# Kernel tuning notes

Hardware: AMD Instinct MI355X
Metric: run time of the kernel (lower is better)

The kernel has to match this reference:

```python
import jax, jax.numpy as jnp
import numpy as np

B, F, S, P, E, H = 64, 32, 512, 96, 8, 2048
TOP_K = 2
ALPHA = 10.0
ENT_EPS = 1e-8
CV_EPS = 1e-10


def setup_inputs() -> dict:
    key = jax.random.key(0)
    ks = jax.random.split(key, 8)
    s = 0.02
    return {
        "x": jax.random.normal(ks[0], (B, F, S), dtype=jnp.float32),
        "time_embedding": jax.random.normal(ks[1], (B, F, S), dtype=jnp.float32),
        "Wg": jax.random.normal(ks[2], (S, E), dtype=jnp.float32) * s,
        "bg": jnp.zeros((E,), dtype=jnp.float32),
        "W1": jax.random.normal(ks[3], (E, S, H), dtype=jnp.float32) * s,
        "b1": jnp.zeros((E, H), dtype=jnp.float32),
        "W2": jax.random.normal(ks[4], (E, H, P), dtype=jnp.float32) * s,
        "b2": jnp.zeros((E, P), dtype=jnp.float32),
    }


def _gates(tf, Wg, bg):
    # tf: [F, B, S] -> logits [F, B, E]
    logits = jnp.einsum('fbs,se->fbe', tf, Wg) + bg
    # kthvalue(x, E - top_k + 1) = (E - top_k)-th entry (0-based) of ascending sort = k-th largest
    kth = jnp.sort(logits, axis=-1)[..., E - TOP_K]  # [F, B]
    mask = logits < kth[..., None]
    sm = jax.nn.softmax(logits, axis=-1)
    dec = jnp.where(mask, ALPHA * jnp.log(sm + 1.0), ALPHA * (jnp.exp(sm) - 1.0))
    return jax.nn.softmax(dec, axis=-1)  # [F, B, E]


def reference(x, time_embedding, Wg, bg, W1, b1, W2, b2):
    xf = jnp.transpose(x, (1, 0, 2))               # [F, B, S]
    tf = jnp.transpose(time_embedding, (1, 0, 2))  # [F, B, S]
    gates = _gates(tf, Wg, bg)                     # [F, B, E]

    # all experts on all features (eval mode: dropout = identity)
    h = jax.nn.gelu(jnp.einsum('fbs,esh->febh', xf, W1) + b1[None, :, None, :], approximate=False)
    eo = jnp.einsum('febh,ehp->febp', h, W2) + b2[None, :, None, :]  # [F, E, B, P]
    out = jnp.einsum('fbe,febp->fbp', gates, eo)   # gated weighted sum
    output = jnp.transpose(out, (1, 0, 2))         # [B, F, P]

    # selector loss: cv_squared of importance = gates.sum(batch) expanded over pred_len
    gsum = gates.sum(axis=1)                       # [F, E]
    imp = jnp.broadcast_to(gsum[..., None], (F, E, P)).reshape(F, E * P)
    cv = jnp.var(imp, axis=1, ddof=1) / (jnp.mean(imp, axis=1) ** 2 + CV_EPS)
    selector_loss = jnp.sum(cv)                    # loss_coef = 1.0

    # entropy loss: importance1 = gates.mean(batch) expanded over pred_len
    gmean = gates.mean(axis=1)                     # [F, E]
    imp1 = jnp.broadcast_to(gmean[..., None], (F, E, P))
    entropy_loss = jnp.sum((-imp1 * jnp.log(imp1 + ENT_EPS)).mean(axis=(1, 2)))

    return output, selector_loss, entropy_loss
```

## Files before the change

kernel.cpp:

```cpp
#include <hip/hip_runtime.h>
#include <math.h>

#define B_ 64
#define F_ 32
#define S_ 512
#define P_ 96
#define E_ 8
#define H_ 2048
#define M_ 2048

#define BM 128
#define BH 128
#define BK 64
#define ZSPLIT 4
#define HPZ (H_ / ZSPLIT)
#define NHT (HPZ / BH)
#define NKC (S_ / BK)
#define HPITCH 136

typedef __bf16 bf16x8 __attribute__((ext_vector_type(8)));
typedef __bf16 bf16x4 __attribute__((ext_vector_type(4)));
typedef float f32x4 __attribute__((ext_vector_type(4)));

#define MFMA16(a, b, c) __builtin_amdgcn_mfma_f32_16x16x32_bf16((a), (b), (c), 0, 0, 0)

#define GLL16(gp, lp) __builtin_amdgcn_global_load_lds(                     \
    (const __attribute__((address_space(1))) void*)(gp),                    \
    (__attribute__((address_space(3))) void*)(lp), 16, 0, 0)

__device__ __forceinline__ float fast_gelu(float x) {
  float e = __builtin_amdgcn_exp2f(-2.45546696f * x);
  return x * __builtin_amdgcn_rcpf(1.0f + e);
}

__global__ __launch_bounds__(256) void k_prep_w1(const float* __restrict__ W1,
                                                 __bf16* __restrict__ w1t) {
  __shared__ __align__(16) __bf16 btile[256 * 68];
  const int tid = threadIdx.x;
  int e = blockIdx.x >> 5, hstrip = blockIdx.x & 31;
  const float* src = W1 + (size_t)e * S_ * H_ + hstrip * 64;
  __bf16* dstb = w1t + (size_t)e * H_ * S_ + (size_t)(hstrip * 64) * S_;
#pragma unroll
  for (int pass = 0; pass < 2; ++pass) {
    {
      int rb = tid >> 2;
      int hseg = (tid & 3) * 16;
#pragma unroll
      for (int it = 0; it < 4; ++it) {
        int r = it * 64 + rb;
        const float* srow = src + (size_t)(pass * 256 + r) * H_ + hseg;
#pragma unroll
        for (int k = 0; k < 4; ++k) {
          f32x4 v = *(const f32x4*)(srow + k * 4);
          bf16x4 o = {(__bf16)v[0], (__bf16)v[1], (__bf16)v[2], (__bf16)v[3]};
          *(bf16x4*)&btile[r * 68 + hseg + k * 4] = o;
        }
      }
    }
    __syncthreads();
    {
      int h = tid >> 2;
      int sseg = (tid & 3) * 64;
      __bf16* drow = dstb + (size_t)h * S_ + pass * 256 + sseg;
#pragma unroll
      for (int g = 0; g < 8; ++g) {
        bf16x8 o;
#pragma unroll
        for (int j = 0; j < 8; ++j) o[j] = btile[(sseg + g * 8 + j) * 68 + h];
        *(bf16x8*)(drow + g * 8) = o;
      }
    }
    __syncthreads();
  }
}

__global__ __launch_bounds__(256) void k_prep_rest(const float* __restrict__ x,
                                                   const float* __restrict__ te,
                                                   const float* __restrict__ Wg,
                                                   const float* __restrict__ bg,
                                                   const float* __restrict__ W2,
                                                   __bf16* __restrict__ xbf,
                                                   __bf16* __restrict__ w2t,
                                                   float* __restrict__ gates) {
  __shared__ float tile[64 * 49];
  const int blk = blockIdx.x;
  const int tid = threadIdx.x;

  if (blk < 512) {
    int e = blk >> 6, hi = (blk >> 1) & 31, ph = blk & 1;
    const float* src = W2 + (size_t)e * H_ * P_ + (size_t)(hi * 64) * P_ + ph * 48;
    {
      int h = tid & 63;
      int seg = tid >> 6;
#pragma unroll
      for (int k = 0; k < 3; ++k) {
        f32x4 v = *(const f32x4*)(src + (size_t)h * P_ + seg * 12 + k * 4);
#pragma unroll
        for (int u = 0; u < 4; ++u) tile[h * 49 + seg * 12 + k * 4 + u] = v[u];
      }
    }
    __syncthreads();
    if (tid < 192) {
      int p = tid >> 2;
      int hb = (tid & 3) * 16;
      __bf16* dst = w2t + (size_t)e * P_ * H_ + (size_t)(ph * 48 + p) * H_ + hi * 64 + hb;
      bf16x8 o0, o1;
#pragma unroll
      for (int k = 0; k < 8; ++k) o0[k] = (__bf16)tile[(hb + k) * 49 + p];
#pragma unroll
      for (int k = 0; k < 8; ++k) o1[k] = (__bf16)tile[(hb + 8 + k) * 49 + p];
      *(bf16x8*)dst = o0;
      *(bf16x8*)(dst + 8) = o1;
    }
    return;
  }
  if (blk < 1024) {
    size_t i = (size_t)(blk - 512) * 2048 + (size_t)tid * 8;
#pragma unroll
    for (int k = 0; k < 2; ++k) {
      f32x4 v = *(const f32x4*)(x + i + k * 4);
      bf16x4 o = {(__bf16)v[0], (__bf16)v[1], (__bf16)v[2], (__bf16)v[3]};
      *(bf16x4*)(xbf + i + k * 4) = o;
    }
    return;
  }
  int wave = tid >> 6, lane = tid & 63;
  int m = (blk - 1024) * 4 + wave;
  const float* trow = te + (size_t)m * S_;
  float acc[E_];
#pragma unroll
  for (int e = 0; e < E_; ++e) acc[e] = 0.f;
  for (int s = lane; s < S_; s += 64) {
    float t = trow[s];
    const f32x4* wgr = (const f32x4*)(Wg + s * E_);
    f32x4 a = wgr[0], b = wgr[1];
    acc[0] += t * a[0]; acc[1] += t * a[1]; acc[2] += t * a[2]; acc[3] += t * a[3];
    acc[4] += t * b[0]; acc[5] += t * b[1]; acc[6] += t * b[2]; acc[7] += t * b[3];
  }
#pragma unroll
  for (int e = 0; e < E_; ++e) {
#pragma unroll
    for (int off = 32; off > 0; off >>= 1) acc[e] += __shfl_xor(acc[e], off, 64);
  }
  if (lane == 0) {
    float lg[E_];
    float m1 = -3.4e38f, m2 = -3.4e38f;
#pragma unroll
    for (int e = 0; e < E_; ++e) {
      float v = acc[e] + bg[e];
      lg[e] = v;
      if (v > m1) { m2 = m1; m1 = v; }
      else if (v > m2) { m2 = v; }
    }
    float den = 0.f, sm[E_];
#pragma unroll
    for (int e = 0; e < E_; ++e) { sm[e] = expf(lg[e] - m1); den += sm[e]; }
    float inv = 1.f / den;
    float dmax = -3.4e38f, dec[E_];
#pragma unroll
    for (int e = 0; e < E_; ++e) {
      float p = sm[e] * inv;
      float d = (lg[e] < m2) ? (10.f * logf(p + 1.f)) : (10.f * (expf(p) - 1.f));
      dec[e] = d;
      dmax = fmaxf(dmax, d);
    }
    float dden = 0.f;
#pragma unroll
    for (int e = 0; e < E_; ++e) { dec[e] = expf(dec[e] - dmax); dden += dec[e]; }
    float dinv = 1.f / dden;
#pragma unroll
    for (int e = 0; e < E_; ++e) gates[m * E_ + e] = dec[e] * dinv;
  }
}

__global__ __launch_bounds__(512, 4) void k_experts(
    const __bf16* __restrict__ xbf,
    const __bf16* __restrict__ w1t,
    const __bf16* __restrict__ w2t,
    const float* __restrict__ b1,
    const float* __restrict__ b2,
    const float* __restrict__ gates,
    float* __restrict__ out)
{
  __shared__ __align__(16) __bf16 W1s[BH * BK];
  __shared__ __align__(16) __bf16 Xs[BM * BK];
  __shared__ __align__(16) __bf16 Hs[BM * HPITCH];

  const int tid = threadIdx.x;

  if (blockIdx.z == ZSPLIT) {
    if (blockIdx.x != 0 || blockIdx.y != 0) return;
    float* gsum = (float*)&Hs[0];
    float* cvs  = gsum + F_ * E_;
    float* ents = cvs + F_;
    if (tid < 256) {
      int f = tid >> 3, e = tid & 7;
      float s = 0.f;
      for (int b = 0; b < B_; ++b) s += gates[(size_t)(b * F_ + f) * E_ + e];
      gsum[f * E_ + e] = s;
    }
    __syncthreads();
    if (tid < F_) {
      float mean = 0.f;
#pragma unroll
      for (int k = 0; k < E_; ++k) mean += gsum[tid * E_ + k];
      mean *= (1.f / E_);
      float ss = 0.f;
#pragma unroll
      for (int k = 0; k < E_; ++k) { float d = gsum[tid * E_ + k] - mean; ss += d * d; }
      float var = (float)P_ * ss / (float)(E_ * P_ - 1);
      cvs[tid] = var / (mean * mean + 1e-10f);
      float ent = 0.f;
#pragma unroll
      for (int k = 0; k < E_; ++k) { float g = gsum[tid * E_ + k] * (1.f / B_); ent += -g * logf(g + 1e-8f); }
      ents[tid] = ent * (1.f / E_);
    }
    __syncthreads();
    if (tid == 0) {
      float a = 0.f, b = 0.f;
      for (int k = 0; k < F_; ++k) { a += cvs[k]; b += ents[k]; }
      out[(size_t)M_ * P_ + 0] = a;
      out[(size_t)M_ * P_ + 1] = b;
    }
    return;
  }

  const int wave = tid >> 6, lane = tid & 63;
  const int l15 = lane & 15, quad = lane >> 4;
  const int e = blockIdx.x;
  const int m0 = blockIdx.y * BM;
  const int hz = blockIdx.z * HPZ;

  const int sg = lane & 7;
  const int srl = lane >> 3;
  const int gcol = ((sg ^ srl) * 8);

  const __bf16* xg = xbf + (size_t)(m0 + wave * 8 + srl) * S_ + gcol;
  const __bf16* w1base = w1t + ((size_t)e * H_ + hz + wave * 8 + srl) * S_ + gcol;
  const __bf16* w2z = w2t + (size_t)e * P_ * H_ + hz;

  const int hq = (wave & 3) * 32;
  const int mq = (wave >> 2) * 64;
  const int mt = wave & 3;
  const int ph = wave >> 2;

  const f32x4 fz = {0.f, 0.f, 0.f, 0.f};
  f32x4 acc2[2][3];
#pragma unroll
  for (int rt = 0; rt < 2; ++rt)
#pragma unroll
    for (int j = 0; j < 3; ++j) acc2[rt][j] = fz;

  for (int ht = 0; ht < NHT; ++ht) {
    const __bf16* w1g = w1base + (size_t)(ht * BH) * S_;
    f32x4 acc1[2][4];
#pragma unroll
    for (int i = 0; i < 2; ++i)
#pragma unroll
      for (int j = 0; j < 4; ++j) acc1[i][j] = fz;

    for (int kc = 0; kc < NKC; ++kc) {
#pragma unroll
      for (int p = 0; p < 2; ++p) {
        GLL16(w1g + (size_t)(p * 64) * S_ + kc * BK, &W1s[(p * 64 + wave * 8) * BK]);
        GLL16(xg  + (size_t)(p * 64) * S_ + kc * BK, &Xs[(p * 64 + wave * 8) * BK]);
      }
      __syncthreads();
#pragma unroll
      for (int kk = 0; kk < 2; ++kk) {
        bf16x8 a[2], b[4];
#pragma unroll
        for (int i = 0; i < 2; ++i) {
          int r = hq + i * 16 + l15;
          int g = kk * 4 + quad;
          a[i] = *(const bf16x8*)&W1s[r * BK + ((g ^ (r & 7)) * 8)];
        }
#pragma unroll
        for (int j = 0; j < 4; ++j) {
          int r = mq + j * 16 + l15;
          int g = kk * 4 + quad;
          b[j] = *(const bf16x8*)&Xs[r * BK + ((g ^ (r & 7)) * 8)];
        }
#pragma unroll
        for (int i = 0; i < 2; ++i)
#pragma unroll
          for (int j = 0; j < 4; ++j)
            acc1[i][j] = MFMA16(a[i], b[j], acc1[i][j]);
      }
      __syncthreads();
    }

    {
      const float* b1w = b1 + (size_t)e * H_ + hz + ht * BH + hq;
#pragma unroll
      for (int i = 0; i < 2; ++i) {
        f32x4 bv = *(const f32x4*)(b1w + i * 16 + quad * 4);
#pragma unroll
        for (int j = 0; j < 4; ++j) {
          bf16x4 hv;
#pragma unroll
          for (int r = 0; r < 4; ++r)
            hv[r] = (__bf16)fast_gelu(acc1[i][j][r] + bv[r]);
          *(bf16x4*)&Hs[(mq + j * 16 + l15) * HPITCH + hq + i * 16 + quad * 4] = hv;
        }
      }
    }
    __syncthreads();

    {
      const __bf16* w2c = w2z + ht * BH;
#pragma unroll
      for (int kk = 0; kk < 4; ++kk) {
        bf16x8 a0 = *(const bf16x8*)&Hs[(mt * 32 + l15) * HPITCH + kk * 32 + quad * 8];
        bf16x8 a1 = *(const bf16x8*)&Hs[(mt * 32 + 16 + l15) * HPITCH + kk * 32 + quad * 8];
#pragma unroll
        for (int j = 0; j < 3; ++j) {
          bf16x8 b = *(const bf16x8*)(w2c + (size_t)(ph * 48 + j * 16 + l15) * H_ + kk * 32 + quad * 8);
          acc2[0][j] = MFMA16(a0, b, acc2[0][j]);
          acc2[1][j] = MFMA16(a1, b, acc2[1][j]);
        }
      }
    }
  }

#pragma unroll
  for (int rt = 0; rt < 2; ++rt) {
#pragma unroll
    for (int r = 0; r < 4; ++r) {
      int m = m0 + mt * 32 + rt * 16 + quad * 4 + r;
      float g = gates[m * E_ + e];
#pragma unroll
      for (int j = 0; j < 3; ++j) {
        int col = ph * 48 + j * 16 + l15;
        float v = acc2[rt][j][r];
        if (blockIdx.z == 0) v += b2[e * P_ + col];
        atomicAdd(&out[(size_t)m * P_ + col], g * v);
      }
    }
  }
}

extern "C" void kernel_launch(void* const* d_in, const int* in_sizes, int n_in,
                              void* d_out, int out_size, void* d_ws, size_t ws_size,
                              hipStream_t stream) {
  const float* x  = (const float*)d_in[0];
  const float* te = (const float*)d_in[1];
  const float* Wg = (const float*)d_in[2];
  const float* bg = (const float*)d_in[3];
  const float* W1 = (const float*)d_in[4];
  const float* b1 = (const float*)d_in[5];
  const float* W2 = (const float*)d_in[6];
  const float* b2 = (const float*)d_in[7];
  float* out = (float*)d_out;

  char* ws = (char*)d_ws;
  float* gates = (float*)ws;
  __bf16* xbf  = (__bf16*)(ws + 65536);
  __bf16* w1t  = (__bf16*)(ws + 65536 + 2097152);
  __bf16* w2t  = (__bf16*)(ws + 65536 + 2097152 + 16777216);

  hipMemsetAsync(d_out, 0, (size_t)out_size * sizeof(float), stream);
  k_prep_w1<<<256, 256, 0, stream>>>(W1, w1t);
  k_prep_rest<<<1536, 256, 0, stream>>>(x, te, Wg, bg, W2, xbf, w2t, gates);
  k_experts<<<dim3(E_, M_ / BM, ZSPLIT + 1), 512, 0, stream>>>(xbf, w1t, w2t, b1, b2, gates, out);
}
```

Before: 194.2 us.

## Quantize first expert GEMM inputs to FP8 and use FP8 MFMA

Converts x and W1 to FP8 (W1 pre-scaled by 8) in the prep kernels instead of bf16, and runs the first expert matmul with FP8 16x16x32 MFMA, descaling before GELU. This halves the bytes for the W1/x staging and global-to-LDS loads and uses the higher-throughput FP8 matrix path. LDS tiles shrink, the swizzle and load mapping are redone for byte elements, and launch bounds now target 6 blocks per SM. The trade-off is reduced numerical precision in the first GEMM, which could push outputs past tolerance.

```diff
diff --git a/kernel.cpp b/kernel.cpp
--- a/kernel.cpp
+++ b/kernel.cpp
@@ -17,29 +17,38 @@
 #define NHT (HPZ / BH)
 #define NKC (S_ / BK)
 #define HPITCH 136
+#define W1SCALE 8.0f
 
 typedef __bf16 bf16x8 __attribute__((ext_vector_type(8)));
 typedef __bf16 bf16x4 __attribute__((ext_vector_type(4)));
 typedef float f32x4 __attribute__((ext_vector_type(4)));
+typedef unsigned char u8;
+typedef int i32x2 __attribute__((ext_vector_type(2)));
 
 #define MFMA16(a, b, c) __builtin_amdgcn_mfma_f32_16x16x32_bf16((a), (b), (c), 0, 0, 0)
+#define MFMA8(a, b, c) __builtin_amdgcn_mfma_f32_16x16x32_fp8_fp8((a), (b), (c), 0, 0, 0)
 
 #define GLL16(gp, lp) __builtin_amdgcn_global_load_lds(                     \
     (const __attribute__((address_space(1))) void*)(gp),                    \
     (__attribute__((address_space(3))) void*)(lp), 16, 0, 0)
 
+__device__ __forceinline__ int pk_fp8x4(float a, float b, float c, float d) {
+  int v = __builtin_amdgcn_cvt_pk_fp8_f32(a, b, 0, false);
+  return __builtin_amdgcn_cvt_pk_fp8_f32(c, d, v, true);
+}
+
 __device__ __forceinline__ float fast_gelu(float x) {
   float e = __builtin_amdgcn_exp2f(-2.45546696f * x);
   return x * __builtin_amdgcn_rcpf(1.0f + e);
 }
 
 __global__ __launch_bounds__(256) void k_prep_w1(const float* __restrict__ W1,
-                                                 __bf16* __restrict__ w1t) {
+                                                 u8* __restrict__ w1q) {
   __shared__ __align__(16) __bf16 btile[256 * 68];
   const int tid = threadIdx.x;
   int e = blockIdx.x >> 5, hstrip = blockIdx.x & 31;
   const float* src = W1 + (size_t)e * S_ * H_ + hstrip * 64;
-  __bf16* dstb = w1t + (size_t)e * H_ * S_ + (size_t)(hstrip * 64) * S_;
+  u8* dstb = w1q + (size_t)e * H_ * S_ + (size_t)(hstrip * 64) * S_;
 #pragma unroll
   for (int pass = 0; pass < 2; ++pass) {
     {
@@ -61,13 +70,15 @@
     {
       int h = tid >> 2;
       int sseg = (tid & 3) * 64;
-      __bf16* drow = dstb + (size_t)h * S_ + pass * 256 + sseg;
+      u8* drow = dstb + (size_t)h * S_ + pass * 256 + sseg;
 #pragma unroll
       for (int g = 0; g < 8; ++g) {
-        bf16x8 o;
-#pragma unroll
-        for (int j = 0; j < 8; ++j) o[j] = btile[(sseg + g * 8 + j) * 68 + h];
-        *(bf16x8*)(drow + g * 8) = o;
+        float v[8];
+#pragma unroll
+        for (int j = 0; j < 8; ++j)
+          v[j] = W1SCALE * (float)btile[(sseg + g * 8 + j) * 68 + h];
+        i32x2 o = {pk_fp8x4(v[0], v[1], v[2], v[3]), pk_fp8x4(v[4], v[5], v[6], v[7])};
+        *(i32x2*)(drow + g * 8) = o;
       }
     }
     __syncthreads();
@@ -79,7 +90,7 @@
                                                    const float* __restrict__ Wg,
                                                    const float* __restrict__ bg,
                                                    const float* __restrict__ W2,
-                                                   __bf16* __restrict__ xbf,
+                                                   u8* __restrict__ xq,
                                                    __bf16* __restrict__ w2t,
                                                    float* __restrict__ gates) {
   __shared__ float tile[64 * 49];
@@ -116,12 +127,10 @@
   }
   if (blk < 1024) {
     size_t i = (size_t)(blk - 512) * 2048 + (size_t)tid * 8;
-#pragma unroll
-    for (int k = 0; k < 2; ++k) {
-      f32x4 v = *(const f32x4*)(x + i + k * 4);
-      bf16x4 o = {(__bf16)v[0], (__bf16)v[1], (__bf16)v[2], (__bf16)v[3]};
-      *(bf16x4*)(xbf + i + k * 4) = o;
-    }
+    f32x4 a = *(const f32x4*)(x + i);
+    f32x4 b = *(const f32x4*)(x + i + 4);
+    i32x2 o = {pk_fp8x4(a[0], a[1], a[2], a[3]), pk_fp8x4(b[0], b[1], b[2], b[3])};
+    *(i32x2*)(xq + i) = o;
     return;
   }
   int wave = tid >> 6, lane = tid & 63;
@@ -173,17 +182,17 @@
   }
 }
 
-__global__ __launch_bounds__(512, 4) void k_experts(
-    const __bf16* __restrict__ xbf,
-    const __bf16* __restrict__ w1t,
+__global__ __launch_bounds__(512, 6) void k_experts(
+    const u8* __restrict__ xq,
+    const u8* __restrict__ w1q,
     const __bf16* __restrict__ w2t,
     const float* __restrict__ b1,
     const float* __restrict__ b2,
     const float* __restrict__ gates,
     float* __restrict__ out)
 {
-  __shared__ __align__(16) __bf16 W1s[BH * BK];
-  __shared__ __align__(16) __bf16 Xs[BM * BK];
+  __shared__ __align__(16) u8 W1s[BH * BK];
+  __shared__ __align__(16) u8 Xs[BM * BK];
   __shared__ __align__(16) __bf16 Hs[BM * HPITCH];
 
   const int tid = threadIdx.x;
@@ -231,12 +240,11 @@
   const int m0 = blockIdx.y * BM;
   const int hz = blockIdx.z * HPZ;
 
-  const int sg = lane & 7;
-  const int srl = lane >> 3;
-  const int gcol = ((sg ^ srl) * 8);
-
-  const __bf16* xg = xbf + (size_t)(m0 + wave * 8 + srl) * S_ + gcol;
-  const __bf16* w1base = w1t + ((size_t)e * H_ + hz + wave * 8 + srl) * S_ + gcol;
+  const int srow = tid >> 2;
+  const int spr = tid & 3;
+  const int scol = ((spr ^ (srow & 3)) * 16);
+  const u8* xgp = xq + (size_t)(m0 + srow) * S_ + scol;
+  const u8* w1gp = w1q + ((size_t)e * H_ + hz + srow) * S_ + scol;
   const __bf16* w2z = w2t + (size_t)e * P_ * H_ + hz;
 
   const int hq = (wave & 3) * 32;
@@ -252,7 +260,7 @@
     for (int j = 0; j < 3; ++j) acc2[rt][j] = fz;
 
   for (int ht = 0; ht < NHT; ++ht) {
-    const __bf16* w1g = w1base + (size_t)(ht * BH) * S_;
+    const u8* w1g = w1gp + (size_t)(ht * BH) * S_;
     f32x4 acc1[2][4];
 #pragma unroll
     for (int i = 0; i < 2; ++i)
@@ -260,32 +268,29 @@
       for (int j = 0; j < 4; ++j) acc1[i][j] = fz;
 
     for (int kc = 0; kc < NKC; ++kc) {
-#pragma unroll
-      for (int p = 0; p < 2; ++p) {
-        GLL16(w1g + (size_t)(p * 64) * S_ + kc * BK, &W1s[(p * 64 + wave * 8) * BK]);
-        GLL16(xg  + (size_t)(p * 64) * S_ + kc * BK, &Xs[(p * 64 + wave * 8) * BK]);
-      }
+      GLL16(w1g + kc * BK, &W1s[tid * 16]);
+      GLL16(xgp + kc * BK, &Xs[tid * 16]);
       __syncthreads();
 #pragma unroll
       for (int kk = 0; kk < 2; ++kk) {
-        bf16x8 a[2], b[4];
+        long a[2], b[4];
 #pragma unroll
         for (int i = 0; i < 2; ++i) {
           int r = hq + i * 16 + l15;
-          int g = kk * 4 + quad;
-          a[i] = *(const bf16x8*)&W1s[r * BK + ((g ^ (r & 7)) * 8)];
+          int G = kk * 4 + quad;
+          a[i] = *(const long*)&W1s[r * BK + (((G >> 1) ^ (r & 3)) * 16 + (G & 1) * 8)];
         }
 #pragma unroll
         for (int j = 0; j < 4; ++j) {
           int r = mq + j * 16 + l15;
-          int g = kk * 4 + quad;
-          b[j] = *(const bf16x8*)&Xs[r * BK + ((g ^ (r & 7)) * 8)];
+          int G = kk * 4 + quad;
+          b[j] = *(const long*)&Xs[r * BK + (((G >> 1) ^ (r & 3)) * 16 + (G & 1) * 8)];
         }
 #pragma unroll
         for (int i = 0; i < 2; ++i)
 #pragma unroll
           for (int j = 0; j < 4; ++j)
-            acc1[i][j] = MFMA16(a[i], b[j], acc1[i][j]);
+            acc1[i][j] = MFMA8(a[i], b[j], acc1[i][j]);
       }
       __syncthreads();
     }
@@ -300,7 +305,7 @@
           bf16x4 hv;
 #pragma unroll
           for (int r = 0; r < 4; ++r)
-            hv[r] = (__bf16)fast_gelu(acc1[i][j][r] + bv[r]);
+            hv[r] = (__bf16)fast_gelu(acc1[i][j][r] * (1.0f / W1SCALE) + bv[r]);
           *(bf16x4*)&Hs[(mq + j * 16 + l15) * HPITCH + hq + i * 16 + quad * 4] = hv;
         }
       }
@@ -355,12 +360,12 @@
 
   char* ws = (char*)d_ws;
   float* gates = (float*)ws;
-  __bf16* xbf  = (__bf16*)(ws + 65536);
-  __bf16* w1t  = (__bf16*)(ws + 65536 + 2097152);
-  __bf16* w2t  = (__bf16*)(ws + 65536 + 2097152 + 16777216);
+  u8* xq       = (u8*)(ws + 65536);
+  u8* w1q      = (u8*)(ws + 65536 + 1048576);
+  __bf16* w2t  = (__bf16*)(ws + 65536 + 1048576 + 8388608);
 
   hipMemsetAsync(d_out, 0, (size_t)out_size * sizeof(float), stream);
-  k_prep_w1<<<256, 256, 0, stream>>>(W1, w1t);
-  k_prep_rest<<<1536, 256, 0, stream>>>(x, te, Wg, bg, W2, xbf, w2t, gates);
-  k_experts<<<dim3(E_, M_ / BM, ZSPLIT + 1), 512, 0, stream>>>(xbf, w1t, w2t, b1, b2, gates, out);
-}
+  k_prep_w1<<<256, 256, 0, stream>>>(W1, w1q);
+  k_prep_rest<<<1536, 256, 0, stream>>>(x, te, Wg, bg, W2, xq, w2t, gates);
+  k_experts<<<dim3(E_, M_ / BM, ZSPLIT + 1), 512, 0, stream>>>(xq, w1q, w2t, b1, b2, gates, out);
+}
```

New measurement: 240.1 us. 1.24x slower.
